# Performance work log

Hardware: AMD Instinct MI355X
Metric: run time of the kernel (lower is better)

Reference implementation:

```python
import jax, jax.numpy as jnp
import numpy as np


def _fracdiff(X, alpha):
    """Fractional differencing (1-L)^alpha applied per batch/channel.
    X: (B, T, n), alpha: (B, n) >= 0. Weights w_0 = 1, w_k = w_{k-1}*(k-1-alpha)/k.
    Y[b, t, i] = sum_{k=0..t} w[b, k, i] * X[b, t-k, i]  (causal filter).
    Computed as a linear convolution via FFT (same math, O(T log T)).
    """
    B, T, n = X.shape
    k = jnp.arange(1, T, dtype=X.dtype)[None, :, None]          # (1, T-1, 1)
    factors = (k - 1.0 - alpha[:, None, :]) / k                  # (B, T-1, n)
    w = jnp.concatenate(
        [jnp.ones((B, 1, n), X.dtype), jnp.cumprod(factors, axis=1)], axis=1
    )                                                            # (B, T, n)
    L = 2 * T  # zero-pad to avoid circular wrap-around
    Xf = jnp.fft.rfft(X, n=L, axis=1)
    Wf = jnp.fft.rfft(w, n=L, axis=1)
    Y = jnp.fft.irfft(Xf * Wf, n=L, axis=1)[:, :T, :]
    return Y.astype(X.dtype)


def setup_inputs() -> dict:
    key = jax.random.key(0)
    kx, ka, kA = jax.random.split(key, 3)
    B, T, n = 8, 8192, 128
    X = jax.random.normal(kx, (B, T, n), dtype=jnp.float32)
    # normalize per trial/channel, mirroring normalize_data=True in __init__
    X = (X - X.mean(axis=1, keepdims=True)) / X.std(axis=1, keepdims=True, ddof=1)
    alpha = jax.random.uniform(ka, (B, n), dtype=jnp.float32)
    A = jax.random.normal(kA, (B, n, n), dtype=jnp.float32) * 0.1
    return {"X": X, "alpha": alpha, "A": A}


def reference(X, alpha, A):
    # _resid(): Y = fracdiff(X, relu(alpha)); E = Y[:,1:,:] - X[:,:-1,:] @ A^T
    Y = _fracdiff(X, jax.nn.relu(alpha))
    Yhat = jnp.einsum('bti,bji->btj', X[:, :-1, :], A)  # bmm(X, A.transpose(1,2))
    return Y[:, 1:, :] - Yhat
```

## Files before the change

kernel.cpp:

```cpp
#include <hip/hip_runtime.h>

#define T 8192
#define NCH 128
#define NB 8
#define NS (NB * NCH)
#define TM1 (T - 1)

typedef __bf16 v8bf __attribute__((ext_vector_type(8)));
typedef float v16f __attribute__((ext_vector_type(16)));

#define WREV_LEN 8448
#define WREV_COPY_STRIDE ((size_t)NS * WREV_LEN)

#define ILIM_TRUNC 144
#define KCHUNKS 19
#define WR_D_MIN 2880
#define KMAX_W 2559
#define NW 2560

struct __attribute__((packed, aligned(4))) U16 { uint4 v; };
struct __attribute__((packed, aligned(4))) F16V { float4 v; };

__device__ __forceinline__ uint bf_bits(float f) {
  union { float f; uint u; } v; v.f = f;
  return (v.u + 0x7FFFu + ((v.u >> 16) & 1u)) >> 16;
}

__device__ __forceinline__ uint wbits(const float* wsh, int k) {
  if ((unsigned)k > (unsigned)KMAX_W) return 0u;
  return bf_bits(wsh[k + (k >> 5)]);
}

__global__ __launch_bounds__(256) void wkern(const float* __restrict__ alpha,
                                             ushort* __restrict__ wr2) {
  const int sid = blockIdx.x;
  const float a = fmaxf(alpha[sid], 0.f);
  const int j = threadIdx.x;
  __shared__ float sc[256];
  __shared__ float wsh[NW + NW / 32];
  const int k0 = j * 10;
  float c = 1.f;
  #pragma unroll
  for (int s = 1; s <= 10; ++s) {
    const float k = (float)(k0 + s);
    c *= (k - 1.f - a) / k;
  }
  sc[j] = c;
  __syncthreads();
  for (int off = 1; off < 256; off <<= 1) {
    const float u = (j >= off) ? sc[j - off] : 1.f;
    const float v = sc[j];
    __syncthreads();
    sc[j] = u * v;
    __syncthreads();
  }
  float p = (j == 0) ? 1.f : sc[j - 1];
  wsh[k0 + (k0 >> 5)] = p;
  #pragma unroll
  for (int s = 1; s < 10; ++s) {
    const float k = (float)(k0 + s);
    p *= (k - 1.f - a) / k;
    const int kk = k0 + s;
    wsh[kk + (kk >> 5)] = p;
  }
  __syncthreads();
  uint* c0u = (uint*)(wr2 + (size_t)sid * WREV_LEN);
  uint* c1u = (uint*)(wr2 + WREV_COPY_STRIDE + (size_t)sid * WREV_LEN);
  for (int d = WR_D_MIN + j; d < WREV_LEN / 2; d += 256) {
    const int z = 2 * d;
    const uint a0 = wbits(wsh, 8319 - z);
    const uint a1 = wbits(wsh, 8318 - z);
    const uint a2 = wbits(wsh, 8317 - z);
    c0u[d] = a0 | (a1 << 16);
    c1u[d] = a1 | (a2 << 16);
  }
}

__global__ __launch_bounds__(256) void tkern(const float* __restrict__ X,
                                             ushort* __restrict__ xT) {
  __shared__ ushort tl[64][76];
  const int b = blockIdx.z;
  const int i0 = blockIdx.y << 6;
  const int t0 = blockIdx.x << 6;
  const int f  = threadIdx.x & 15;
  const int tr = threadIdx.x >> 4;
  #pragma unroll
  for (int p = 0; p < 4; ++p) {
    const int tt = tr + (p << 4);
    const float4 v =
        *(const float4*)(X + ((size_t)b * T + t0 + tt) * NCH + i0 + 4 * f);
    tl[4 * f + 0][tt] = (ushort)bf_bits(v.x);
    tl[4 * f + 1][tt] = (ushort)bf_bits(v.y);
    tl[4 * f + 2][tt] = (ushort)bf_bits(v.z);
    tl[4 * f + 3][tt] = (ushort)bf_bits(v.w);
  }
  __syncthreads();
  const int c  = threadIdx.x & 7;
  const int ib = threadIdx.x >> 3;
  #pragma unroll
  for (int p = 0; p < 2; ++p) {
    const int i = ib + (p << 5);
    const uint2 lo = *(const uint2*)&tl[i][8 * c];
    const uint2 hi = *(const uint2*)&tl[i][8 * c + 4];
    const uint4 pk = make_uint4(lo.x, lo.y, hi.x, hi.y);
    *(uint4*)(xT + ((size_t)(b * NCH + i0 + i)) * T + t0 + 8 * c) = pk;
  }
}

__global__ __launch_bounds__(256, 2) void convk(const ushort* __restrict__ wr2,
                                                const ushort* __restrict__ xT,
                                                float* __restrict__ yT) {
  const int sid = blockIdx.x;
  const int tid = threadIdx.x;
  const int wave = tid >> 6;
  const int lane = tid & 63;
  const int ln31 = lane & 31;
  const int q = lane >> 5;

  __shared__ uint4 arena16[1280];

  {
    const int u = tid;
    arena16[((u & 7) * 160) + (u >> 3)] = make_uint4(0, 0, 0, 0);
  }
  {
    const uint4* xg16 = (const uint4*)(xT + (size_t)sid * T);
    for (int u0 = tid; u0 < 1024; u0 += 256) {
      const int u = u0 + 256;
      arena16[((u & 7) * 160) + (u >> 3)] = xg16[u0];
    }
  }
  __syncthreads();

  v16f acc[4][2];
  #pragma unroll
  for (int cc = 0; cc < 4; ++cc)
    #pragma unroll
    for (int rt = 0; rt < 2; ++rt)
      #pragma unroll
      for (int e = 0; e < 16; ++e) acc[cc][rt][e] = 0.f;

  const int s0_par = (8303 - ln31 + 8 * q) & 1;
  const uint* wu = (const uint*)(wr2 + (s0_par ? WREV_COPY_STRIDE : 0) +
                                 (size_t)sid * WREV_LEN);

  uint4 av[10];
  int dw0;
  {
    const int ibase0 = -4 + wave * 8;
    const int s0 = 8303 - 16 * ibase0 - ln31 + 8 * q;
    dw0 = (s0 - s0_par) >> 1;
    #pragma unroll
    for (int j2 = 0; j2 < 10; ++j2)
      av[j2] = ((const U16*)(wu + (dw0 - 8 * j2)))->v;
  }

  for (int K = wave; K < KCHUNKS; K += 4) {
    const int ibase = -4 + K * 8;
    const int dw0n = dw0 - 256;
    const bool more = (K + 4) < KCHUNKS;
    uint4 pf0, pf1, pf2, pf3;
    if (more) {
      pf0 = ((const U16*)(wu + dw0n))->v;
      pf1 = ((const U16*)(wu + (dw0n - 8)))->v;
      pf2 = ((const U16*)(wu + (dw0n - 16)))->v;
      pf3 = ((const U16*)(wu + (dw0n - 24)))->v;
    }
    #pragma unroll
    for (int ii = 0; ii < 8; ++ii) {
      const int i = ibase + ii;
      const v8bf A0 = __builtin_bit_cast(v8bf, av[ii]);
      const v8bf A1 = __builtin_bit_cast(v8bf, av[ii + 2]);
      const int m2 = -2 * (i + 1);
      const int u70 = m2 & 7;
      const int u71 = (m2 + 1) & 7;
      const int G0 = u70 * 160 + 32 + ((m2 - u70) >> 3);
      const int G1 = u71 * 160 + 32 + ((m2 + 1 - u71) >> 3);
      const int phi = ln31 + (q ? G1 : G0);
      #pragma unroll
      for (int cc = 0; cc < 4; ++cc) {
        if (i < (cc == 0 ? 128 : ILIM_TRUNC)) {
          const uint4 bv = arena16[phi + 32 * cc];
          const v8bf Bf = __builtin_bit_cast(v8bf, bv);
          acc[cc][0] = __builtin_amdgcn_mfma_f32_32x32x16_bf16(A0, Bf, acc[cc][0], 0, 0, 0);
          acc[cc][1] = __builtin_amdgcn_mfma_f32_32x32x16_bf16(A1, Bf, acc[cc][1], 0, 0, 0);
        }
      }
    }
    if (more) {
      av[0] = pf0; av[1] = pf1; av[2] = pf2; av[3] = pf3;
      #pragma unroll
      for (int j2 = 4; j2 < 10; ++j2)
        av[j2] = ((const U16*)(wu + (dw0n - 8 * j2)))->v;
    }
    dw0 = dw0n;
  }

  float* const zbase = (float*)arena16;
  const int rowq = 4 * q;
  #pragma unroll
  for (int cc = 0; cc < 4; ++cc) {
    #pragma unroll
    for (int rt = 0; rt < 2; ++rt) {
      __syncthreads();
      float* zone = zbase + wave * 1152;
      #pragma unroll
      for (int g = 0; g < 4; ++g) {
        float4 v = make_float4(acc[cc][rt][4 * g], acc[cc][rt][4 * g + 1],
                               acc[cc][rt][4 * g + 2], acc[cc][rt][4 * g + 3]);
        *(float4*)(zone + ln31 * 36 + 8 * g + rowq) = v;
      }
      __syncthreads();
      const int n2 = tid & 31, rg = tid >> 5;
      const int zi = n2 * 36 + 4 * rg;
      float4 s0 = *(const float4*)(zbase + 0 * 1152 + zi);
      float4 s1 = *(const float4*)(zbase + 1 * 1152 + zi);
      float4 s2 = *(const float4*)(zbase + 2 * 1152 + zi);
      float4 s3 = *(const float4*)(zbase + 3 * 1152 + zi);
      float4 s;
      s.x = s0.x + s1.x + s2.x + s3.x;
      s.y = s0.y + s1.y + s2.y + s3.y;
      s.z = s0.z + s1.z + s2.z + s3.z;
      s.w = s0.w + s1.w + s2.w + s3.w;
      *(float4*)(yT + (size_t)sid * T + 2048 * cc + 64 * n2 + 32 * rt + 4 * rg) = s;
    }
  }
}

__global__ __launch_bounds__(256) void outk(const float* __restrict__ X,
                                            const float* __restrict__ A,
                                            const float* __restrict__ yT,
                                            float* __restrict__ out) {
  const int b = blockIdx.y;
  const int t0 = blockIdx.x << 6;
  const int tid = threadIdx.x;
  const int wave = tid >> 6;
  const int lane = tid & 63;
  const int ln31 = lane & 31;
  const int q = lane >> 5;

  __shared__ uint4 arena[3072];

  {
    const float* Ab = A + (size_t)b * NCH * NCH;
    #pragma unroll
    for (int g = 0; g < 8; ++g) {
      const int u = g * 256 + tid;
      const int jr = u >> 4, c4 = u & 15;
      const float4 f0 = *(const float4*)(Ab + jr * NCH + 8 * c4);
      const float4 f1 = *(const float4*)(Ab + jr * NCH + 8 * c4 + 4);
      uint4 pk;
      pk.x = bf_bits(f0.x) | (bf_bits(f0.y) << 16);
      pk.y = bf_bits(f0.z) | (bf_bits(f0.w) << 16);
      pk.z = bf_bits(f1.x) | (bf_bits(f1.y) << 16);
      pk.w = bf_bits(f1.z) | (bf_bits(f1.w) << 16);
      arena[c4 * 128 + ((jr + c4) & 127)] = pk;
    }
  }
  {
    const float* Xb = X + ((size_t)b * T + t0) * NCH;
    #pragma unroll
    for (int g = 0; g < 4; ++g) {
      const int u = g * 256 + tid;
      const int m = u >> 4, c4 = u & 15;
      const float4 f0 = *(const float4*)(Xb + m * NCH + 8 * c4);
      const float4 f1 = *(const float4*)(Xb + m * NCH + 8 * c4 + 4);
      uint4 pk;
      pk.x = bf_bits(f0.x) | (bf_bits(f0.y) << 16);
      pk.y = bf_bits(f0.z) | (bf_bits(f0.w) << 16);
      pk.z = bf_bits(f1.x) | (bf_bits(f1.y) << 16);
      pk.w = bf_bits(f1.z) | (bf_bits(f1.w) << 16);
      arena[2048 + c4 * 64 + ((m + c4) & 63)] = pk;
    }
  }
  __syncthreads();

  v16f acc[2];
  #pragma unroll
  for (int mt = 0; mt < 2; ++mt)
    #pragma unroll
    for (int e = 0; e < 16; ++e) acc[mt][e] = 0.f;

  const int nt = wave;
  #pragma unroll
  for (int kk = 0; kk < 8; ++kk) {
    const int c4 = 2 * kk + q;
    const uint4 bv = arena[c4 * 128 + ((nt * 32 + ln31 + c4) & 127)];
    const v8bf Bf = __builtin_bit_cast(v8bf, bv);
    #pragma unroll
    for (int mt = 0; mt < 2; ++mt) {
      const uint4 avv = arena[2048 + c4 * 64 + ((mt * 32 + ln31 + c4) & 63)];
      const v8bf Af = __builtin_bit_cast(v8bf, avv);
      acc[mt] = __builtin_amdgcn_mfma_f32_32x32x16_bf16(Af, Bf, acc[mt], 0, 0, 0);
    }
  }

  __syncthreads();
  float* const ldsY = (float*)arena;
  {
    const int jr = tid >> 1, h = tid & 1;
    const float* yr = yT + ((size_t)(b * NCH + jr)) * T + t0 + 1 + 32 * h;
    #pragma unroll
    for (int v = 0; v < 8; ++v) {
      const float4 f = ((const F16V*)(yr + 4 * v))->v;
      const int tt = 32 * h + 4 * v;
      ldsY[(tt + 0) * 132 + jr] = f.x;
      ldsY[(tt + 1) * 132 + jr] = f.y;
      ldsY[(tt + 2) * 132 + jr] = f.z;
      ldsY[(tt + 3) * 132 + jr] = f.w;
    }
  }
  __syncthreads();

  const int jj = nt * 32 + ln31;
  float* og = out + (size_t)b * TM1 * NCH + jj;
  #pragma unroll
  for (int mt = 0; mt < 2; ++mt) {
    #pragma unroll
    for (int g = 0; g < 4; ++g) {
      const int r0 = mt * 32 + 8 * g + 4 * q;
      #pragma unroll
      for (int e = 0; e < 4; ++e) {
        const int t = t0 + r0 + e;
        const float val = ldsY[(r0 + e) * 132 + jj] - acc[mt][4 * g + e];
        if (t < TM1) og[(size_t)t * NCH] = val;
      }
    }
  }
}

extern "C" void kernel_launch(void* const* d_in, const int* in_sizes, int n_in,
                              void* d_out, int out_size, void* d_ws, size_t ws_size,
                              hipStream_t stream) {
  const float* X     = (const float*)d_in[0];
  const float* alpha = (const float*)d_in[1];
  const float* A     = (const float*)d_in[2];
  float* out = (float*)d_out;
  char* ws = (char*)d_ws;

  ushort* wr2 = (ushort*)ws;
  ushort* xT  = (ushort*)(ws + 34603008);
  float*  yT  = (float*)(ws + 34603008 + 16777216);

  hipLaunchKernelGGL(wkern, dim3(NS), dim3(256), 0, stream, alpha, wr2);
  hipLaunchKernelGGL(tkern, dim3(T / 64, NCH / 64, NB), dim3(256), 0, stream, X, xT);
  hipLaunchKernelGGL(convk, dim3(NS), dim3(256), 0, stream, wr2, xT, yT);
  hipLaunchKernelGGL(outk, dim3(T / 64, NB), dim3(256), 0, stream, X, A, yT, out);
}
```

Measured before the change: 149.7 us.

## Restructure convolution MFMA tiling to reuse weight fragments across four row tiles

Changes the conv kernel's MFMA tile mapping from 4 column chunks x 2 row tiles to 2 column groups x 4 row tiles. Each LDS-loaded X fragment pair is now reused by four weight fragments, so LDS reads per MFMA drop. To support this, the LDS layout moves to a 16-way interleave with stride 84, the reversed-weight buffer is padded, and more weight registers are held (14 instead of 10). Boundary masking moves to per-row-tile conditions. The cost is higher register pressure and a shifted K-chunk start, which may add redundant MFMAs at the edges.

```diff
diff --git a/kernel.cpp b/kernel.cpp
--- a/kernel.cpp
+++ b/kernel.cpp
@@ -9,7 +9,7 @@
 typedef __bf16 v8bf __attribute__((ext_vector_type(8)));
 typedef float v16f __attribute__((ext_vector_type(16)));
 
-#define WREV_LEN 8448
+#define WREV_LEN 8512
 #define WREV_COPY_STRIDE ((size_t)NS * WREV_LEN)
 
 #define ILIM_TRUNC 144
@@ -117,46 +117,49 @@
   const int ln31 = lane & 31;
   const int q = lane >> 5;
 
-  __shared__ uint4 arena16[1280];
-
-  {
-    const int u = tid;
-    arena16[((u & 7) * 160) + (u >> 3)] = make_uint4(0, 0, 0, 0);
+  __shared__ uint4 arena16[1344];
+
+  {
+    int u = tid;
+    arena16[84 * (u & 15) + (u >> 4)] = make_uint4(0, 0, 0, 0);
+    if (tid < 64) {
+      u = 256 + tid;
+      arena16[84 * (u & 15) + (u >> 4)] = make_uint4(0, 0, 0, 0);
+    }
   }
   {
     const uint4* xg16 = (const uint4*)(xT + (size_t)sid * T);
     for (int u0 = tid; u0 < 1024; u0 += 256) {
-      const int u = u0 + 256;
-      arena16[((u & 7) * 160) + (u >> 3)] = xg16[u0];
-    }
-  }
-  __syncthreads();
-
-  v16f acc[4][2];
-  #pragma unroll
-  for (int cc = 0; cc < 4; ++cc)
-    #pragma unroll
-    for (int rt = 0; rt < 2; ++rt)
+      const int u = u0 + 320;
+      arena16[84 * (u & 15) + (u >> 4)] = xg16[u0];
+    }
+  }
+  __syncthreads();
+
+  v16f acc[2][4];
+  #pragma unroll
+  for (int g = 0; g < 2; ++g)
+    #pragma unroll
+    for (int rt = 0; rt < 4; ++rt)
       #pragma unroll
-      for (int e = 0; e < 16; ++e) acc[cc][rt][e] = 0.f;
+      for (int e = 0; e < 16; ++e) acc[g][rt][e] = 0.f;
 
   const int s0_par = (8303 - ln31 + 8 * q) & 1;
   const uint* wu = (const uint*)(wr2 + (s0_par ? WREV_COPY_STRIDE : 0) +
                                  (size_t)sid * WREV_LEN);
 
-  uint4 av[10];
+  uint4 av[14];
   int dw0;
   {
-    const int ibase0 = -4 + wave * 8;
-    const int s0 = 8303 - 16 * ibase0 - ln31 + 8 * q;
+    const int s0 = 8495 - 128 * wave - ln31 + 8 * q;
     dw0 = (s0 - s0_par) >> 1;
     #pragma unroll
-    for (int j2 = 0; j2 < 10; ++j2)
+    for (int j2 = 0; j2 < 14; ++j2)
       av[j2] = ((const U16*)(wu + (dw0 - 8 * j2)))->v;
   }
 
-  for (int K = wave; K < KCHUNKS; K += 4) {
-    const int ibase = -4 + K * 8;
+  for (int K = wave - 1; K < KCHUNKS; K += 4) {
+    const int ibase = 8 * K - 4;
     const int dw0n = dw0 - 256;
     const bool more = (K + 4) < KCHUNKS;
     uint4 pf0, pf1, pf2, pf3;
@@ -169,28 +172,30 @@
     #pragma unroll
     for (int ii = 0; ii < 8; ++ii) {
       const int i = ibase + ii;
-      const v8bf A0 = __builtin_bit_cast(v8bf, av[ii]);
-      const v8bf A1 = __builtin_bit_cast(v8bf, av[ii + 2]);
-      const int m2 = -2 * (i + 1);
-      const int u70 = m2 & 7;
-      const int u71 = (m2 + 1) & 7;
-      const int G0 = u70 * 160 + 32 + ((m2 - u70) >> 3);
-      const int G1 = u71 * 160 + 32 + ((m2 + 1 - u71) >> 3);
-      const int phi = ln31 + (q ? G1 : G0);
-      #pragma unroll
-      for (int cc = 0; cc < 4; ++cc) {
-        if (i < (cc == 0 ? 128 : ILIM_TRUNC)) {
-          const uint4 bv = arena16[phi + 32 * cc];
-          const v8bf Bf = __builtin_bit_cast(v8bf, bv);
-          acc[cc][0] = __builtin_amdgcn_mfma_f32_32x32x16_bf16(A0, Bf, acc[cc][0], 0, 0, 0);
-          acc[cc][1] = __builtin_amdgcn_mfma_f32_32x32x16_bf16(A1, Bf, acc[cc][1], 0, 0, 0);
+      if (i >= -9 && i < ILIM_TRUNC) {
+        const int s00 = 320 - 2 * (i + 1);
+        const int s01 = s00 + 1;
+        const int G0 = 84 * (s00 & 15) + (s00 >> 4);
+        const int G1 = 84 * (s01 & 15) + (s01 >> 4);
+        const int phi = ln31 + (q ? G1 : G0);
+        const uint4 bv0 = arena16[phi];
+        const uint4 bv1 = arena16[phi + 32];
+        const v8bf B0 = __builtin_bit_cast(v8bf, bv0);
+        const v8bf B1 = __builtin_bit_cast(v8bf, bv1);
+        #pragma unroll
+        for (int rt = 0; rt < 4; ++rt) {
+          if (i + 2 * rt >= -3) {
+            const v8bf Af = __builtin_bit_cast(v8bf, av[ii + 2 * rt]);
+            acc[0][rt] = __builtin_amdgcn_mfma_f32_32x32x16_bf16(Af, B0, acc[0][rt], 0, 0, 0);
+            acc[1][rt] = __builtin_amdgcn_mfma_f32_32x32x16_bf16(Af, B1, acc[1][rt], 0, 0, 0);
+          }
         }
       }
     }
     if (more) {
       av[0] = pf0; av[1] = pf1; av[2] = pf2; av[3] = pf3;
       #pragma unroll
-      for (int j2 = 4; j2 < 10; ++j2)
+      for (int j2 = 4; j2 < 14; ++j2)
         av[j2] = ((const U16*)(wu + (dw0n - 8 * j2)))->v;
     }
     dw0 = dw0n;
@@ -199,16 +204,16 @@
   float* const zbase = (float*)arena16;
   const int rowq = 4 * q;
   #pragma unroll
-  for (int cc = 0; cc < 4; ++cc) {
-    #pragma unroll
-    for (int rt = 0; rt < 2; ++rt) {
+  for (int g = 0; g < 2; ++g) {
+    #pragma unroll
+    for (int rt = 0; rt < 4; ++rt) {
       __syncthreads();
       float* zone = zbase + wave * 1152;
       #pragma unroll
-      for (int g = 0; g < 4; ++g) {
-        float4 v = make_float4(acc[cc][rt][4 * g], acc[cc][rt][4 * g + 1],
-                               acc[cc][rt][4 * g + 2], acc[cc][rt][4 * g + 3]);
-        *(float4*)(zone + ln31 * 36 + 8 * g + rowq) = v;
+      for (int gg = 0; gg < 4; ++gg) {
+        float4 v = make_float4(acc[g][rt][4 * gg], acc[g][rt][4 * gg + 1],
+                               acc[g][rt][4 * gg + 2], acc[g][rt][4 * gg + 3]);
+        *(float4*)(zone + ln31 * 36 + 8 * gg + rowq) = v;
       }
       __syncthreads();
       const int n2 = tid & 31, rg = tid >> 5;
@@ -222,7 +227,7 @@
       s.y = s0.y + s1.y + s2.y + s3.y;
       s.z = s0.z + s1.z + s2.z + s3.z;
       s.w = s0.w + s1.w + s2.w + s3.w;
-      *(float4*)(yT + (size_t)sid * T + 2048 * cc + 64 * n2 + 32 * rt + 4 * rg) = s;
+      *(float4*)(yT + (size_t)sid * T + 4096 * g + 128 * n2 + 32 * rt + 4 * rg) = s;
     }
   }
 }
@@ -339,8 +344,8 @@
   char* ws = (char*)d_ws;
 
   ushort* wr2 = (ushort*)ws;
-  ushort* xT  = (ushort*)(ws + 34603008);
-  float*  yT  = (float*)(ws + 34603008 + 16777216);
+  ushort* xT  = (ushort*)(ws + 34865152);
+  float*  yT  = (float*)(ws + 34865152 + 16777216);
 
   hipLaunchKernelGGL(wkern, dim3(NS), dim3(256), 0, stream, alpha, wr2);
   hipLaunchKernelGGL(tkern, dim3(T / 64, NCH / 64, NB), dim3(256), 0, stream, X, xT);
```

Result: no change. 148.7 us (-0.7%).
